# Optimization experiments

Hardware: AMD Instinct MI355X
Metric: run time of the kernel (lower is better)

## Reference

```python
import jax, jax.numpy as jnp
import numpy as np

B, Q, C, N_PER, GS = 8, 2048, 256, 64, 8
H1, H2 = 256, 64
EPS = 1e-5


def make_grid():
    a = jnp.linspace(-0.1, 0.1, GS)
    gx, gy = jnp.meshgrid(a, a, indexing='ij')  # torch.meshgrid default 'ij'
    return jnp.stack([gx.reshape(-1), gy.reshape(-1)], axis=1)  # (n, 2)


def setup_inputs() -> dict:
    key = jax.random.key(0)
    ks = jax.random.split(key, 10)
    s = lambda k, shp, fan: jax.random.normal(k, shp, jnp.float32) / np.sqrt(fan)
    return {
        'tokens': jax.random.normal(ks[0], (B, Q, C), jnp.float32),
        'grid': make_grid(),
        'Wc': s(ks[1], (C, 3), C), 'bc': jnp.zeros((3,), jnp.float32),
        'W1': s(ks[2], (C + 2, H1), C + 2), 'b1': jnp.zeros((H1,), jnp.float32),
        'gamma1': jnp.ones((H1,), jnp.float32), 'beta1': jnp.zeros((H1,), jnp.float32),
        'W2': s(ks[3], (H1, H2), H1), 'b2': jnp.zeros((H2,), jnp.float32),
        'gamma2': jnp.ones((H2,), jnp.float32), 'beta2': jnp.zeros((H2,), jnp.float32),
        'W3': s(ks[4], (H2, 3), H2), 'b3': jnp.zeros((3,), jnp.float32),
    }


def batchnorm(x, gamma, beta):
    # BatchNorm1d in training mode: stats over batch (B*Q) and length (n) dims,
    # per channel (last axis here).
    mean = jnp.mean(x, axis=(0, 1, 2), keepdims=True)
    var = jnp.var(x, axis=(0, 1, 2), keepdims=True)
    return gamma * (x - mean) * jax.lax.rsqrt(var + EPS) + beta


def reference(tokens, grid, Wc, bc, W1, b1, gamma1, beta1, W2, b2, gamma2, beta2, W3, b3):
    coarse = tokens @ Wc + bc  # (B, Q, 3)
    # conv1 (1x1) on concat([tokens_expanded, grid]) == split matmul + broadcast add;
    # avoids materializing the (B,Q,n,C+2) concat explicitly.
    tok_part = tokens @ W1[:C]                 # (B, Q, H1)
    grid_part = grid @ W1[C:]                  # (n, H1)
    h = tok_part[:, :, None, :] + grid_part[None, None, :, :] + b1  # (B, Q, n, H1)
    h = jax.nn.relu(batchnorm(h, gamma1, beta1))
    h = jnp.einsum('bqnc,cd->bqnd', h, W2) + b2  # (B, Q, n, H2)
    h = jax.nn.relu(batchnorm(h, gamma2, beta2))
    disp = jnp.einsum('bqnc,cd->bqnd', h, W3) + b3  # (B, Q, n, 3)
    fine = (coarse[:, :, None, :] + disp).reshape(B, Q * N_PER, 3)
    return coarse, fine
```

## Files before the change

kernel.cpp:

```cpp
#include <hip/hip_runtime.h>
#include <hip/hip_bf16.h>

#define ROWS 16384
#define C_   256
#define H1_  256
#define H2_  64
#define EPSN 1e-5f

typedef __bf16 bf16x8 __attribute__((ext_vector_type(8)));
typedef __bf16 bf16x4 __attribute__((ext_vector_type(4)));
typedef __bf16 bf16x2 __attribute__((ext_vector_type(2)));
typedef float  f32x4  __attribute__((ext_vector_type(4)));
typedef float  f32x2  __attribute__((ext_vector_type(2)));

__device__ __forceinline__ bf16x2 cvt2(float a, float b) {
#if __has_builtin(__builtin_amdgcn_cvt_pk_bf16_f32)
    return __builtin_bit_cast(bf16x2, __builtin_amdgcn_cvt_pk_bf16_f32(a, b));
#else
    bf16x2 r; r[0] = (__bf16)a; r[1] = (__bf16)b; return r;
#endif
}

__device__ __forceinline__ void barrier_lgkm() {
    asm volatile("s_waitcnt lgkmcnt(0)" ::: "memory");
    __builtin_amdgcn_sched_barrier(0);
    __builtin_amdgcn_s_barrier();
    __builtin_amdgcn_sched_barrier(0);
}

__global__ __launch_bounds__(256) void k0_pack(const float* __restrict__ W1,
                                               const float* __restrict__ W2,
                                               const float* __restrict__ W3,
                                               const float* __restrict__ grid,
                                               __bf16* __restrict__ W1p,
                                               __bf16* __restrict__ W2p,
                                               __bf16* __restrict__ W3p,
                                               float* __restrict__ zero_base,
                                               float* __restrict__ gm,
                                               float* __restrict__ gvv) {
    __shared__ float gl[128];
    int idx = blockIdx.x * 256 + threadIdx.x;
    if (idx < 65536) {
        int j = idx & 7, l = (idx >> 3) & 63, rest = idx >> 9;
        int ks = rest & 7, CT = rest >> 3;
        int k = ks * 32 + ((l >> 4) << 3) + j;
        int c = CT * 16 + (l & 15);
        W1p[idx] = (__bf16)W1[k * H1_ + c];
    } else {
        int i2 = idx - 65536;
        int j = i2 & 7, l = (i2 >> 3) & 63, rest = i2 >> 9;
        int ks = rest & 7, CK = rest >> 3;
        int k = ks * 32 + ((l >> 4) << 3) + j;
        int c2 = CK * 16 + (l & 15);
        W2p[i2] = (__bf16)W2[k * H2_ + c2];
    }
    if (idx < 1024) {
        int j = idx & 7, l = (idx >> 3) & 63, ks = idx >> 9;
        int k = ks * 32 + ((l >> 4) << 3) + j;
        int c = l & 15;
        W3p[idx] = (c < 3) ? (__bf16)W3[k * 3 + c] : (__bf16)0.f;
    }
    if (idx < 24576) zero_base[idx] = 0.0f;
    if (blockIdx.x == 0) {
        int t = threadIdx.x;
        if (t < 128) gl[t] = grid[t];
        __syncthreads();
        float wx = W1[C_ * H1_ + t];
        float wy = W1[(C_ + 1) * H1_ + t];
        float mg = 0.f, qg = 0.f;
#pragma unroll
        for (int n = 0; n < 64; ++n) {
            float gv = gl[2 * n] * wx + gl[2 * n + 1] * wy;
            mg += gv; qg = fmaf(gv, gv, qg);
        }
        mg *= (1.f / 64.f);
        gm[t] = mg;
        gvv[t] = qg * (1.f / 64.f) - mg * mg;
    }
}

__device__ __forceinline__ void prep_ctx(const float* __restrict__ grid,
                                         const float* __restrict__ W1,
                                         const float* __restrict__ a1p, int c0,
                                         f32x2* wgx2, f32x2* wgy2, float* A_) {
#pragma unroll
    for (int j = 0; j < 8; ++j) A_[j] = grid[2 * j + 1];
    f32x4 a0 = *(const f32x4*)(a1p + c0), a1h = *(const f32x4*)(a1p + c0 + 4);
    f32x4 x0 = *(const f32x4*)(W1 + C_ * H1_ + c0), x1 = *(const f32x4*)(W1 + C_ * H1_ + c0 + 4);
    f32x4 y0 = *(const f32x4*)(W1 + (C_ + 1) * H1_ + c0), yh = *(const f32x4*)(W1 + (C_ + 1) * H1_ + c0 + 4);
    float av[8] = {a0[0], a0[1], a0[2], a0[3], a1h[0], a1h[1], a1h[2], a1h[3]};
    float wx[8] = {x0[0], x0[1], x0[2], x0[3], x1[0], x1[1], x1[2], x1[3]};
    float wy[8] = {y0[0], y0[1], y0[2], y0[3], yh[0], yh[1], yh[2], yh[3]};
#pragma unroll
    for (int e = 0; e < 4; ++e) {
        wgx2[e][0] = av[2 * e] * wx[2 * e];     wgx2[e][1] = av[2 * e + 1] * wx[2 * e + 1];
        wgy2[e][0] = av[2 * e] * wy[2 * e];     wgy2[e][1] = av[2 * e + 1] * wy[2 * e + 1];
    }
}

__device__ __forceinline__ void stage16(__bf16* __restrict__ y1, int nbase, int c0,
                                        f32x4 a0, f32x4 a1h, f32x4 d0, f32x4 d1h,
                                        const f32x2* wgx2, const f32x2* wgy2,
                                        float ax0, float ax1, f32x4 ay4,
                                        f32x4 t0, f32x4 t1) {
    int chunk = c0 >> 3;
    f32x2 base2[4];
    base2[0][0] = fmaf(a0[0], t0[0], d0[0]);  base2[0][1] = fmaf(a0[1], t0[1], d0[1]);
    base2[1][0] = fmaf(a0[2], t0[2], d0[2]);  base2[1][1] = fmaf(a0[3], t0[3], d0[3]);
    base2[2][0] = fmaf(a1h[0], t1[0], d1h[0]); base2[2][1] = fmaf(a1h[1], t1[1], d1h[1]);
    base2[3][0] = fmaf(a1h[2], t1[2], d1h[2]); base2[3][1] = fmaf(a1h[3], t1[3], d1h[3]);
#pragma unroll
    for (int ih = 0; ih < 2; ++ih) {
        float axs = ih ? ax1 : ax0;
        f32x2 ax2 = {axs, axs};
        f32x2 tc2[4];
#pragma unroll
        for (int e = 0; e < 4; ++e) tc2[e] = __builtin_elementwise_fma(wgx2[e], ax2, base2[e]);
#pragma unroll
        for (int kk = 0; kk < 4; ++kk) {
            float ays = ay4[kk];
            f32x2 ay2 = {ays, ays};
            f32x2 z = {0.f, 0.f};
            int n = nbase + ih * 8 + 2 * kk;
            bf16x8 out;
            bf16x2* o2 = (bf16x2*)&out;
#pragma unroll
            for (int e = 0; e < 4; ++e) {
                f32x2 v = __builtin_elementwise_max(
                    __builtin_elementwise_fma(wgy2[e], ay2, tc2[e]), z);
                o2[e] = cvt2(v[0], v[1]);
            }
            *(bf16x8*)(&y1[n * 256 + ((chunk ^ (n & 7)) << 3)]) = out;
        }
    }
}

__global__ __launch_bounds__(256) void k1a(const float* __restrict__ tokens,
                                           const __bf16* __restrict__ W1p,
                                           const float* __restrict__ Wc,
                                           const float* __restrict__ bc,
                                           float* __restrict__ tokpart,
                                           float* __restrict__ coarse,
                                           float* __restrict__ p1s,
                                           float* __restrict__ p1q) {
    __shared__ __align__(16) __bf16 Al[16 * 264];
    int t = threadIdx.x, w = t >> 6, l = t & 63;
    int quad = l >> 4, col = l & 15;
    int rowbase = (blockIdx.x >> 1) * 16;
    int colhalf = blockIdx.x & 1;
    int slot = blockIdx.x & 31;

    bf16x8 bfr[16];
#pragma unroll
    for (int ctl = 0; ctl < 2; ++ctl)
#pragma unroll
        for (int ks = 0; ks < 8; ++ks) {
            int CT = colhalf * 8 + w * 2 + ctl;
            bfr[ctl * 8 + ks] = *(const bf16x8*)(W1p + (((CT * 8 + ks) * 64 + l) * 8));
        }
    {
        int r = t >> 4, cb = (t & 15) * 16;
        const float* src = tokens + (size_t)(rowbase + r) * C_ + cb;
        f32x4 t0 = *(const f32x4*)(src);
        f32x4 t1 = *(const f32x4*)(src + 4);
        f32x4 t2 = *(const f32x4*)(src + 8);
        f32x4 t3 = *(const f32x4*)(src + 12);
        bf16x8 v0, v1;
        bf16x2* p0 = (bf16x2*)&v0; bf16x2* p1 = (bf16x2*)&v1;
        p0[0] = cvt2(t0[0], t0[1]); p0[1] = cvt2(t0[2], t0[3]);
        p0[2] = cvt2(t1[0], t1[1]); p0[3] = cvt2(t1[2], t1[3]);
        p1[0] = cvt2(t2[0], t2[1]); p1[1] = cvt2(t2[2], t2[3]);
        p1[2] = cvt2(t3[0], t3[1]); p1[3] = cvt2(t3[2], t3[3]);
        *(bf16x8*)(&Al[r * 264 + cb]) = v0;
        *(bf16x8*)(&Al[r * 264 + cb + 8]) = v1;
    }
    barrier_lgkm();

    bf16x8 af[8];
#pragma unroll
    for (int ks = 0; ks < 8; ++ks)
        af[ks] = *(const bf16x8*)(&Al[col * 264 + ks * 32 + quad * 8]);

#pragma unroll
    for (int ctl = 0; ctl < 2; ++ctl) {
        f32x4 acc = {0.f, 0.f, 0.f, 0.f};
#pragma unroll
        for (int ks = 0; ks < 8; ++ks)
            acc = __builtin_amdgcn_mfma_f32_16x16x32_bf16(af[ks], bfr[ctl * 8 + ks], acc, 0, 0, 0);
        int c = colhalf * 128 + w * 32 + ctl * 16 + col;
        float s = 0.f, q = 0.f;
#pragma unroll
        for (int rr = 0; rr < 4; ++rr) {
            float v = acc[rr];
            tokpart[(size_t)(rowbase + quad * 4 + rr) * C_ + c] = v;
            s += v; q += v * v;
        }
        s += __shfl_xor(s, 16, 64); s += __shfl_xor(s, 32, 64);
        q += __shfl_xor(q, 16, 64); q += __shfl_xor(q, 32, 64);
        if (l < 16) {
            int cc = colhalf * 128 + w * 32 + ctl * 16 + l;
            atomicAdd(p1s + slot * C_ + cc, s);
            atomicAdd(p1q + slot * C_ + cc, q);
        }
    }
    if (colhalf == 0) {
        const f32x4* wcp = (const f32x4*)(Wc + l * 12);
        f32x4 wa = wcp[0], wb = wcp[1], wv = wcp[2];
        float wcl[12] = {wa[0], wa[1], wa[2], wa[3], wb[0], wb[1], wb[2], wb[3],
                         wv[0], wv[1], wv[2], wv[3]};
#pragma unroll
        for (int rr = 0; rr < 4; ++rr) {
            int r = w * 4 + rr;
            bf16x4 tv4 = *(const bf16x4*)(&Al[r * 264 + l * 4]);
            float p[3] = {0.f, 0.f, 0.f};
#pragma unroll
            for (int i = 0; i < 4; ++i) {
                float tvf = (float)tv4[i];
#pragma unroll
                for (int j = 0; j < 3; ++j) p[j] = fmaf(tvf, wcl[i * 3 + j], p[j]);
            }
#pragma unroll
            for (int off = 1; off < 64; off <<= 1)
#pragma unroll
                for (int j = 0; j < 3; ++j) p[j] += __shfl_xor(p[j], off, 64);
            if (l == 0) {
#pragma unroll
                for (int j = 0; j < 3; ++j)
                    coarse[(size_t)(rowbase + r) * 3 + j] = p[j] + bc[j];
            }
        }
    }
}

__global__ void k1b(const float* __restrict__ gm, const float* __restrict__ gvv,
                    const float* __restrict__ gamma1, const float* __restrict__ beta1,
                    const float* __restrict__ p1s, const float* __restrict__ p1q,
                    float* __restrict__ a1o, float* __restrict__ d1o) {
    int t = threadIdx.x;
    float S = 0.f, Q = 0.f;
#pragma unroll 8
    for (int s = 0; s < 32; ++s) { S += p1s[s * C_ + t]; Q += p1q[s * C_ + t]; }
    float mean_t = S / (float)ROWS;
    float var_t = Q / (float)ROWS - mean_t * mean_t;
    float a1 = gamma1[t] * rsqrtf(var_t + gvv[t] + EPSN);
    a1o[t] = a1;
    d1o[t] = beta1[t] - a1 * (mean_t + gm[t]);
}

template <bool SPILL>
__global__ __launch_bounds__(256) void k2(const float* __restrict__ tokpart,
                                          const float* __restrict__ grid,
                                          const float* __restrict__ W1,
                                          const __bf16* __restrict__ W2p,
                                          const float* __restrict__ a1,
                                          const float* __restrict__ d1,
                                          float* __restrict__ p2s,
                                          float* __restrict__ p2q,
                                          __bf16* __restrict__ h2s) {
    __shared__ __align__(16) __bf16 y1[2][64 * 256];
    int t = threadIdx.x, w = t >> 6, l = t & 63;
    int quad = l >> 4, col = l & 15;
    int wn = w >> 1, wc = w & 1;
    int c0 = (l & 31) * 8, nh = l >> 5;
    int sw = col & 7;

    bf16x8 bfr[16];
#pragma unroll
    for (int ck = 0; ck < 2; ++ck)
#pragma unroll
        for (int ks = 0; ks < 8; ++ks)
            bfr[ck * 8 + ks] = *(const bf16x8*)(W2p + ((((wc * 2 + ck) * 8 + ks) * 64 + l) * 8));

    f32x2 wgx2[4], wgy2[4]; float A_[8];
    prep_ctx(grid, W1, a1, c0, wgx2, wgy2, A_);

    float ax0 = (w & 2) ? ((w & 1) ? A_[6] : A_[4]) : ((w & 1) ? A_[2] : A_[0]);
    float ax1 = (w & 2) ? ((w & 1) ? A_[7] : A_[5]) : ((w & 1) ? A_[3] : A_[1]);
    f32x4 ay4;
    ay4[0] = nh ? A_[1] : A_[0];
    ay4[1] = nh ? A_[3] : A_[2];
    ay4[2] = nh ? A_[5] : A_[4];
    ay4[3] = nh ? A_[7] : A_[6];
    int nbase = w * 16 + nh;

    f32x4 va0 = *(const f32x4*)(a1 + c0), va1h = *(const f32x4*)(a1 + c0 + 4);
    f32x4 vd0 = *(const f32x4*)(d1 + c0), vd1h = *(const f32x4*)(d1 + c0 + 4);

    float s[2][4] = {}, q[2][4] = {};

    const float* tokbase = tokpart + (size_t)blockIdx.x * 8 * C_;
    {
        f32x4 p0 = *(const f32x4*)(tokbase + c0);
        f32x4 p1 = *(const f32x4*)(tokbase + c0 + 4);
        stage16(&y1[0][0], nbase, c0, va0, va1h, vd0, vd1h, wgx2, wgy2, ax0, ax1, ay4, p0, p1);
    }
    f32x4 t0 = *(const f32x4*)(tokbase + C_ + c0);
    f32x4 t1 = *(const f32x4*)(tokbase + C_ + c0 + 4);
    barrier_lgkm();

#pragma unroll 1
    for (int r8 = 0; r8 < 8; ++r8) {
        int row = blockIdx.x * 8 + r8;
        int cur = r8 & 1;
        int nr = (r8 < 6) ? (r8 + 2) : 7;
        f32x4 n0 = *(const f32x4*)(tokbase + (size_t)nr * C_ + c0);
        f32x4 n1 = *(const f32x4*)(tokbase + (size_t)nr * C_ + c0 + 4);

#pragma unroll
        for (int rt = 0; rt < 2; ++rt) {
            int rowb = (wn * 32 + rt * 16 + col) * 256;
            bf16x8 af[8];
#pragma unroll
            for (int ks = 0; ks < 8; ++ks)
                af[ks] = *(const bf16x8*)(&y1[cur][rowb + (((ks * 4 + quad) ^ sw) << 3)]);
#pragma unroll
            for (int ck = 0; ck < 2; ++ck) {
                f32x4 acc = {0.f, 0.f, 0.f, 0.f};
#pragma unroll
                for (int ks = 0; ks < 8; ++ks)
                    acc = __builtin_amdgcn_mfma_f32_16x16x32_bf16(bfr[ck * 8 + ks], af[ks], acc, 0, 0, 0);
#pragma unroll
                for (int rr = 0; rr < 4; ++rr) {
                    s[ck][rr] += acc[rr];
                    q[ck][rr] += acc[rr] * acc[rr];
                }
                if constexpr (SPILL) {
                    bf16x4 v; bf16x2* v2 = (bf16x2*)&v;
                    v2[0] = cvt2(acc[0], acc[1]);
                    v2[1] = cvt2(acc[2], acc[3]);
                    *(bf16x4*)(h2s + (size_t)row * 4096 +
                               ((wn * 2 + rt) * 4 + wc * 2 + ck) * 256 + l * 4) = v;
                }
            }
        }
        if (r8 < 7)
            stage16(&y1[cur ^ 1][0], nbase, c0, va0, va1h, vd0, vd1h,
                    wgx2, wgy2, ax0, ax1, ay4, t0, t1);
        barrier_lgkm();
        t0 = n0; t1 = n1;
    }
    int slot = ((blockIdx.x << 1) | wn) & 63;
#pragma unroll
    for (int ck = 0; ck < 2; ++ck)
#pragma unroll
        for (int rr = 0; rr < 4; ++rr) {
            float sv = s[ck][rr], qv = q[ck][rr];
            sv += __shfl_xor(sv, 1, 64); sv += __shfl_xor(sv, 2, 64);
            sv += __shfl_xor(sv, 4, 64); sv += __shfl_xor(sv, 8, 64);
            qv += __shfl_xor(qv, 1, 64); qv += __shfl_xor(qv, 2, 64);
            qv += __shfl_xor(qv, 4, 64); qv += __shfl_xor(qv, 8, 64);
            if (col == 0) {
                int c2 = wc * 32 + ck * 16 + quad * 4 + rr;
                atomicAdd(p2s + slot * H2_ + c2, sv);
                atomicAdd(p2q + slot * H2_ + c2, qv);
            }
        }
}

__global__ void k2b(const float* __restrict__ p2s, const float* __restrict__ p2q,
                    const float* __restrict__ gamma2, const float* __restrict__ beta2,
                    float* __restrict__ a2o, float* __restrict__ d2o) {
    int t = threadIdx.x;
    float S = 0.f, Q = 0.f;
#pragma unroll 8
    for (int s = 0; s < 64; ++s) { S += p2s[s * H2_ + t]; Q += p2q[s * H2_ + t]; }
    const float invN = 1.f / ((float)ROWS * 64.f);
    float mean = S * invN;
    float var = Q * invN - mean * mean;
    float a2 = gamma2[t] * rsqrtf(var + EPSN);
    a2o[t] = a2;
    d2o[t] = beta2[t] - a2 * mean;
}

__global__ __launch_bounds__(256) void k3s(const __bf16* __restrict__ h2s,
                                           const float* __restrict__ a2,
                                           const float* __restrict__ d2p,
                                           const __bf16* __restrict__ W3p,
                                           const float* __restrict__ b3,
                                           const float* __restrict__ coarse,
                                           float* __restrict__ fine) {
    __shared__ __align__(16) __bf16 y2l[4][16 * 64];
    __shared__ __align__(16) float finebuf[8 * 192];
    int t = threadIdx.x, w = t >> 6, l = t & 63;
    int quad = l >> 4, col = l & 15;
    int sw = col & 7;

    bf16x8 wfr[2];
#pragma unroll
    for (int ks = 0; ks < 2; ++ks)
        wfr[ks] = *(const bf16x8*)(W3p + ((ks * 64 + l) * 8));

    float a2v[16], d2v[16];
#pragma unroll
    for (int ck = 0; ck < 4; ++ck)
#pragma unroll
        for (int rr = 0; rr < 4; ++rr) {
            int c2 = ck * 16 + quad * 4 + rr;
            a2v[ck * 4 + rr] = a2[c2];
            d2v[ck * 4 + rr] = d2p[c2];
        }
    float b3v = (col < 3) ? b3[col] : 0.f;
    __bf16* yw = &y2l[w][0];

#pragma unroll 1
    for (int r8 = 0; r8 < 8; ++r8) {
        int row = blockIdx.x * 8 + r8;
        const __bf16* src = h2s + (size_t)row * 4096 + l * 4;
        bf16x4 u[4];
#pragma unroll
        for (int ck = 0; ck < 4; ++ck)
            u[ck] = *(const bf16x4*)(src + (w * 4 + ck) * 256);
#pragma unroll
        for (int ck = 0; ck < 4; ++ck) {
            float y0 = fmaxf(fmaf(a2v[ck * 4 + 0], (float)u[ck][0], d2v[ck * 4 + 0]), 0.f);
            float y1v = fmaxf(fmaf(a2v[ck * 4 + 1], (float)u[ck][1], d2v[ck * 4 + 1]), 0.f);
            float y2 = fmaxf(fmaf(a2v[ck * 4 + 2], (float)u[ck][2], d2v[ck * 4 + 2]), 0.f);
            float y3 = fmaxf(fmaf(a2v[ck * 4 + 3], (float)u[ck][3], d2v[ck * 4 + 3]), 0.f);
            bf16x4 v; bf16x2* v2 = (bf16x2*)&v;
            v2[0] = cvt2(y0, y1v); v2[1] = cvt2(y2, y3);
            int chunk = ck * 2 + (quad >> 1);
            *(bf16x4*)(&yw[col * 64 + ((chunk ^ sw) << 3) + (quad & 1) * 4]) = v;
        }
        bf16x8 af2[2];
#pragma unroll
        for (int ks = 0; ks < 2; ++ks)
            af2[ks] = *(const bf16x8*)(&yw[col * 64 + (((ks * 4 + quad) ^ sw) << 3)]);
        f32x4 acc = {0.f, 0.f, 0.f, 0.f};
        acc = __builtin_amdgcn_mfma_f32_16x16x32_bf16(af2[0], wfr[0], acc, 0, 0, 0);
        acc = __builtin_amdgcn_mfma_f32_16x16x32_bf16(af2[1], wfr[1], acc, 0, 0, 0);
        if (col < 3) {
            float cj = coarse[row * 3 + col] + b3v;
#pragma unroll
            for (int rr = 0; rr < 4; ++rr)
                finebuf[r8 * 192 + (w * 16 + quad * 4 + rr) * 3 + col] = acc[rr] + cj;
        }
    }
    __syncthreads();
    {
        float* dst = fine + (size_t)blockIdx.x * 1536;
        const f32x4* fb = (const f32x4*)finebuf;
        *(f32x4*)(dst + 4 * t) = fb[t];
        if (t < 128) *(f32x4*)(dst + 1024 + 4 * t) = fb[256 + t];
    }
}

__global__ __launch_bounds__(256) void k3r(const float* __restrict__ tokpart,
                                           const float* __restrict__ grid,
                                           const float* __restrict__ W1,
                                           const __bf16* __restrict__ W2p,
                                           const float* __restrict__ a1,
                                           const float* __restrict__ d1,
                                           const __bf16* __restrict__ W3p,
                                           const float* __restrict__ a2,
                                           const float* __restrict__ d2p,
                                           const float* __restrict__ b3,
                                           const float* __restrict__ coarse,
                                           float* __restrict__ fine) {
    __shared__ __align__(16) __bf16 y1[64 * 256];
    __shared__ __align__(16) __bf16 y2l[64 * 72];
    __shared__ __align__(16) float finebuf[8 * 192];
    int t = threadIdx.x, w = t >> 6, l = t & 63;
    int quad = l >> 4, col = l & 15;
    int wn = w >> 1, wc = w & 1;
    int c0 = (l & 31) * 8, nh = l >> 5;
    int sw = col & 7;

    bf16x8 bfr[16];
#pragma unroll
    for (int ck = 0; ck < 2; ++ck)
#pragma unroll
        for (int ks = 0; ks < 8; ++ks)
            bfr[ck * 8 + ks] = *(const bf16x8*)(W2p + ((((wc * 2 + ck) * 8 + ks) * 64 + l) * 8));
    bf16x8 wfr[2];
#pragma unroll
    for (int ks = 0; ks < 2; ++ks)
        wfr[ks] = *(const bf16x8*)(W3p + ((ks * 64 + l) * 8));

    f32x2 wgx2[4], wgy2[4]; float A_[8];
    prep_ctx(grid, W1, a1, c0, wgx2, wgy2, A_);

    float ax0 = (w & 2) ? ((w & 1) ? A_[6] : A_[4]) : ((w & 1) ? A_[2] : A_[0]);
    float ax1 = (w & 2) ? ((w & 1) ? A_[7] : A_[5]) : ((w & 1) ? A_[3] : A_[1]);
    f32x4 ay4;
    ay4[0] = nh ? A_[1] : A_[0];
    ay4[1] = nh ? A_[3] : A_[2];
    ay4[2] = nh ? A_[5] : A_[4];
    ay4[3] = nh ? A_[7] : A_[6];
    int nbase = w * 16 + nh;

    f32x4 va0 = *(const f32x4*)(a1 + c0), va1h = *(const f32x4*)(a1 + c0 + 4);
    f32x4 vd0 = *(const f32x4*)(d1 + c0), vd1h = *(const f32x4*)(d1 + c0 + 4);

    float a2v[8], d2v[8];
#pragma unroll
    for (int ck = 0; ck < 2; ++ck)
#pragma unroll
        for (int rr = 0; rr < 4; ++rr) {
            int c2 = wc * 32 + ck * 16 + quad * 4 + rr;
            a2v[ck * 4 + rr] = a2[c2];
            d2v[ck * 4 + rr] = d2p[c2];
        }
    float b3v = (col < 3) ? b3[col] : 0.f;

    const float* tokbase = tokpart + (size_t)blockIdx.x * 8 * C_;
    f32x4 t0 = *(const f32x4*)(tokbase + c0);
    f32x4 t1 = *(const f32x4*)(tokbase + c0 + 4);

#pragma unroll 1
    for (int r8 = 0; r8 < 8; ++r8) {
        int row = blockIdx.x * 8 + r8;
        int nr = (r8 < 7) ? (r8 + 1) : 7;
        f32x4 n0 = *(const f32x4*)(tokbase + (size_t)nr * C_ + c0);
        f32x4 n1 = *(const f32x4*)(tokbase + (size_t)nr * C_ + c0 + 4);

        stage16(y1, nbase, c0, va0, va1h, vd0, vd1h, wgx2, wgy2, ax0, ax1, ay4, t0, t1);
        barrier_lgkm();
#pragma unroll
        for (int rt = 0; rt < 2; ++rt) {
            int rowb = (wn * 32 + rt * 16 + col) * 256;
            bf16x8 af[8];
#pragma unroll
            for (int ks = 0; ks < 8; ++ks)
                af[ks] = *(const bf16x8*)(&y1[rowb + (((ks * 4 + quad) ^ sw) << 3)]);
#pragma unroll
            for (int ck = 0; ck < 2; ++ck) {
                f32x4 acc = {0.f, 0.f, 0.f, 0.f};
#pragma unroll
                for (int ks = 0; ks < 8; ++ks)
                    acc = __builtin_amdgcn_mfma_f32_16x16x32_bf16(bfr[ck * 8 + ks], af[ks], acc, 0, 0, 0);
                bf16x4 v; bf16x2* v2 = (bf16x2*)&v;
                float y0 = fmaxf(fmaf(a2v[ck * 4 + 0], acc[0], d2v[ck * 4 + 0]), 0.f);
                float y1v = fmaxf(fmaf(a2v[ck * 4 + 1], acc[1], d2v[ck * 4 + 1]), 0.f);
                float y2 = fmaxf(fmaf(a2v[ck * 4 + 2], acc[2], d2v[ck * 4 + 2]), 0.f);
                float y3 = fmaxf(fmaf(a2v[ck * 4 + 3], acc[3], d2v[ck * 4 + 3]), 0.f);
                v2[0] = cvt2(y0, y1v); v2[1] = cvt2(y2, y3);
                *(bf16x4*)(&y2l[(wn * 32 + rt * 16 + col) * 72 + wc * 32 + ck * 16 + quad * 4]) = v;
            }
        }
        barrier_lgkm();
        bf16x8 af2[2];
#pragma unroll
        for (int ks = 0; ks < 2; ++ks)
            af2[ks] = *(const bf16x8*)(&y2l[(w * 16 + col) * 72 + ks * 32 + quad * 8]);
        f32x4 d2acc = {0.f, 0.f, 0.f, 0.f};
        d2acc = __builtin_amdgcn_mfma_f32_16x16x32_bf16(af2[0], wfr[0], d2acc, 0, 0, 0);
        d2acc = __builtin_amdgcn_mfma_f32_16x16x32_bf16(af2[1], wfr[1], d2acc, 0, 0, 0);
        if (col < 3) {
            float cj = coarse[row * 3 + col] + b3v;
#pragma unroll
            for (int rr = 0; rr < 4; ++rr)
                finebuf[r8 * 192 + (w * 16 + quad * 4 + rr) * 3 + col] = d2acc[rr] + cj;
        }
        barrier_lgkm();
        t0 = n0; t1 = n1;
    }
    {
        float* dst = fine + (size_t)blockIdx.x * 1536;
        const f32x4* fb = (const f32x4*)finebuf;
        *(f32x4*)(dst + 4 * t) = fb[t];
        if (t < 128) *(f32x4*)(dst + 1024 + 4 * t) = fb[256 + t];
    }
}

extern "C" void kernel_launch(void* const* d_in, const int* in_sizes, int n_in,
                              void* d_out, int out_size, void* d_ws, size_t ws_size,
                              hipStream_t stream) {
    (void)in_sizes; (void)n_in; (void)out_size;
    const float* tokens = (const float*)d_in[0];
    const float* grid   = (const float*)d_in[1];
    const float* Wc     = (const float*)d_in[2];
    const float* bc     = (const float*)d_in[3];
    const float* W1     = (const float*)d_in[4];
    const float* gamma1 = (const float*)d_in[6];
    const float* beta1  = (const float*)d_in[7];
    const float* W2     = (const float*)d_in[8];
    const float* gamma2 = (const float*)d_in[10];
    const float* beta2  = (const float*)d_in[11];
    const float* W3     = (const float*)d_in[12];
    const float* b3     = (const float*)d_in[13];

    char* ws = (char*)d_ws;
    __bf16* W1p     = (__bf16*)(ws);
    __bf16* W2p     = (__bf16*)(ws + 131072);
    float*  p1s     = (float*)(ws + 163840);
    float*  p1q     = (float*)(ws + 196608);
    float*  p2s     = (float*)(ws + 229376);
    float*  p2q     = (float*)(ws + 245760);
    float*  a1      = (float*)(ws + 262144);
    float*  d1      = (float*)(ws + 263168);
    float*  a2      = (float*)(ws + 264192);
    float*  d2p     = (float*)(ws + 264448);
    __bf16* W3p     = (__bf16*)(ws + 264704);
    float*  gm      = (float*)(ws + 266752);
    float*  gvv     = (float*)(ws + 267776);
    float*  tokpart = (float*)(ws + 268800);
    __bf16* h2s     = (__bf16*)(ws + 17046016);

    const size_t SPILL_NEED = 17046016ull + 134217728ull;
    bool spill = ws_size >= SPILL_NEED;

    float* coarse = (float*)d_out;
    float* fine   = (float*)d_out + (size_t)ROWS * 3;

    k0_pack<<<320, 256, 0, stream>>>(W1, W2, W3, grid, W1p, W2p, W3p, p1s, gm, gvv);
    k1a<<<2048, 256, 0, stream>>>(tokens, W1p, Wc, bc, tokpart, coarse, p1s, p1q);
    k1b<<<1, 256, 0, stream>>>(gm, gvv, gamma1, beta1, p1s, p1q, a1, d1);
    if (spill) {
        k2<true><<<ROWS / 8, 256, 0, stream>>>(tokpart, grid, W1, W2p, a1, d1,
                                               p2s, p2q, h2s);
        k2b<<<1, 64, 0, stream>>>(p2s, p2q, gamma2, beta2, a2, d2p);
        k3s<<<ROWS / 8, 256, 0, stream>>>(h2s, a2, d2p, W3p, b3, coarse, fine);
    } else {
        k2<false><<<ROWS / 8, 256, 0, stream>>>(tokpart, grid, W1, W2p, a1, d1,
                                                p2s, p2q, h2s);
        k2b<<<1, 64, 0, stream>>>(p2s, p2q, gamma2, beta2, a2, d2p);
        k3r<<<ROWS / 8, 256, 0, stream>>>(tokpart, grid, W1, W2p, a1, d1,
                                          W3p, a2, d2p, b3, coarse, fine);
    }
}
```

Before: 195.4 us.

## Process 64 rows per k1a block and compute coarse head via MFMA

k1a now handles 64 token rows per block instead of 16, so each block reuses its register-resident W1 fragments across four row groups and the grid shrinks from 2048 to 512 blocks. BN1 partial sums are accumulated in registers across row groups before the atomics, which cuts atomic traffic. The coarse projection (tokens @ Wc) moves from scalar FMAs plus a 64-lane shuffle reduction to an MFMA against a zero-padded bf16 Wc packed in k0_pack. The trade-offs are fewer blocks for latency hiding and larger shared memory per block, and coarse is now computed from bf16-rounded weights.

```diff
diff --git a/kernel.cpp b/kernel.cpp
--- a/kernel.cpp
+++ b/kernel.cpp
@@ -31,10 +31,12 @@
 __global__ __launch_bounds__(256) void k0_pack(const float* __restrict__ W1,
                                                const float* __restrict__ W2,
                                                const float* __restrict__ W3,
+                                               const float* __restrict__ Wc,
                                                const float* __restrict__ grid,
                                                __bf16* __restrict__ W1p,
                                                __bf16* __restrict__ W2p,
                                                __bf16* __restrict__ W3p,
+                                               __bf16* __restrict__ Wcp,
                                                float* __restrict__ zero_base,
                                                float* __restrict__ gm,
                                                float* __restrict__ gvv) {
@@ -60,6 +62,12 @@
         int c = l & 15;
         W3p[idx] = (c < 3) ? (__bf16)W3[k * 3 + c] : (__bf16)0.f;
     }
+    if (idx < 4096) {
+        int j = idx & 7, l = (idx >> 3) & 63, ks = idx >> 9;
+        int k = ks * 32 + ((l >> 4) << 3) + j;
+        int c = l & 15;
+        Wcp[idx] = (c < 3) ? (__bf16)Wc[k * 3 + c] : (__bf16)0.f;
+    }
     if (idx < 24576) zero_base[idx] = 0.0f;
     if (blockIdx.x == 0) {
         int t = threadIdx.x;
@@ -137,17 +145,18 @@
 
 __global__ __launch_bounds__(256) void k1a(const float* __restrict__ tokens,
                                            const __bf16* __restrict__ W1p,
-                                           const float* __restrict__ Wc,
+                                           const __bf16* __restrict__ Wcp,
                                            const float* __restrict__ bc,
                                            float* __restrict__ tokpart,
                                            float* __restrict__ coarse,
                                            float* __restrict__ p1s,
                                            float* __restrict__ p1q) {
-    __shared__ __align__(16) __bf16 Al[16 * 264];
+    __shared__ __align__(16) __bf16 Al[64 * 264];
     int t = threadIdx.x, w = t >> 6, l = t & 63;
     int quad = l >> 4, col = l & 15;
-    int rowbase = (blockIdx.x >> 1) * 16;
+    int group = blockIdx.x >> 1;
     int colhalf = blockIdx.x & 1;
+    int rowbase = group * 64;
     int slot = blockIdx.x & 31;
 
     bf16x8 bfr[16];
@@ -158,8 +167,17 @@
             int CT = colhalf * 8 + w * 2 + ctl;
             bfr[ctl * 8 + ks] = *(const bf16x8*)(W1p + (((CT * 8 + ks) * 64 + l) * 8));
         }
-    {
-        int r = t >> 4, cb = (t & 15) * 16;
+    bf16x8 cfr[8];
+    if (colhalf == 0) {
+#pragma unroll
+        for (int ks = 0; ks < 8; ++ks)
+            cfr[ks] = *(const bf16x8*)(Wcp + ((ks * 64 + l) * 8));
+    }
+    float bcv = (col < 3) ? bc[col] : 0.f;
+
+#pragma unroll
+    for (int rg = 0; rg < 4; ++rg) {
+        int r = rg * 16 + (t >> 4), cb = (t & 15) * 16;
         const float* src = tokens + (size_t)(rowbase + r) * C_ + cb;
         f32x4 t0 = *(const f32x4*)(src);
         f32x4 t1 = *(const f32x4*)(src + 4);
@@ -176,58 +194,52 @@
     }
     barrier_lgkm();
 
-    bf16x8 af[8];
-#pragma unroll
-    for (int ks = 0; ks < 8; ++ks)
-        af[ks] = *(const bf16x8*)(&Al[col * 264 + ks * 32 + quad * 8]);
+    float s[2] = {0.f, 0.f}, q[2] = {0.f, 0.f};
+
+#pragma unroll
+    for (int rg = 0; rg < 4; ++rg) {
+        int rb16 = rg * 16;
+        bf16x8 af[8];
+#pragma unroll
+        for (int ks = 0; ks < 8; ++ks)
+            af[ks] = *(const bf16x8*)(&Al[(rb16 + col) * 264 + ks * 32 + quad * 8]);
+
+#pragma unroll
+        for (int ctl = 0; ctl < 2; ++ctl) {
+            f32x4 acc = {0.f, 0.f, 0.f, 0.f};
+#pragma unroll
+            for (int ks = 0; ks < 8; ++ks)
+                acc = __builtin_amdgcn_mfma_f32_16x16x32_bf16(af[ks], bfr[ctl * 8 + ks], acc, 0, 0, 0);
+            int c = colhalf * 128 + w * 32 + ctl * 16 + col;
+#pragma unroll
+            for (int rr = 0; rr < 4; ++rr) {
+                float v = acc[rr];
+                tokpart[(size_t)(rowbase + rb16 + quad * 4 + rr) * C_ + c] = v;
+                s[ctl] += v; q[ctl] += v * v;
+            }
+        }
+        if (colhalf == 0) {
+            f32x4 cacc = {0.f, 0.f, 0.f, 0.f};
+#pragma unroll
+            for (int ks = 0; ks < 8; ++ks)
+                cacc = __builtin_amdgcn_mfma_f32_16x16x32_bf16(af[ks], cfr[ks], cacc, 0, 0, 0);
+            if (col < 3) {
+#pragma unroll
+                for (int rr = 0; rr < 4; ++rr)
+                    coarse[(size_t)(rowbase + rb16 + quad * 4 + rr) * 3 + col] = cacc[rr] + bcv;
+            }
+        }
+    }
 
 #pragma unroll
     for (int ctl = 0; ctl < 2; ++ctl) {
-        f32x4 acc = {0.f, 0.f, 0.f, 0.f};
-#pragma unroll
-        for (int ks = 0; ks < 8; ++ks)
-            acc = __builtin_amdgcn_mfma_f32_16x16x32_bf16(af[ks], bfr[ctl * 8 + ks], acc, 0, 0, 0);
-        int c = colhalf * 128 + w * 32 + ctl * 16 + col;
-        float s = 0.f, q = 0.f;
-#pragma unroll
-        for (int rr = 0; rr < 4; ++rr) {
-            float v = acc[rr];
-            tokpart[(size_t)(rowbase + quad * 4 + rr) * C_ + c] = v;
-            s += v; q += v * v;
-        }
-        s += __shfl_xor(s, 16, 64); s += __shfl_xor(s, 32, 64);
-        q += __shfl_xor(q, 16, 64); q += __shfl_xor(q, 32, 64);
+        float sv = s[ctl], qv = q[ctl];
+        sv += __shfl_xor(sv, 16, 64); sv += __shfl_xor(sv, 32, 64);
+        qv += __shfl_xor(qv, 16, 64); qv += __shfl_xor(qv, 32, 64);
         if (l < 16) {
             int cc = colhalf * 128 + w * 32 + ctl * 16 + l;
-            atomicAdd(p1s + slot * C_ + cc, s);
-            atomicAdd(p1q + slot * C_ + cc, q);
-        }
-    }
-    if (colhalf == 0) {
-        const f32x4* wcp = (const f32x4*)(Wc + l * 12);
-        f32x4 wa = wcp[0], wb = wcp[1], wv = wcp[2];
-        float wcl[12] = {wa[0], wa[1], wa[2], wa[3], wb[0], wb[1], wb[2], wb[3],
-                         wv[0], wv[1], wv[2], wv[3]};
-#pragma unroll
-        for (int rr = 0; rr < 4; ++rr) {
-            int r = w * 4 + rr;
-            bf16x4 tv4 = *(const bf16x4*)(&Al[r * 264 + l * 4]);
-            float p[3] = {0.f, 0.f, 0.f};
-#pragma unroll
-            for (int i = 0; i < 4; ++i) {
-                float tvf = (float)tv4[i];
-#pragma unroll
-                for (int j = 0; j < 3; ++j) p[j] = fmaf(tvf, wcl[i * 3 + j], p[j]);
-            }
-#pragma unroll
-            for (int off = 1; off < 64; off <<= 1)
-#pragma unroll
-                for (int j = 0; j < 3; ++j) p[j] += __shfl_xor(p[j], off, 64);
-            if (l == 0) {
-#pragma unroll
-                for (int j = 0; j < 3; ++j)
-                    coarse[(size_t)(rowbase + r) * 3 + j] = p[j] + bc[j];
-            }
+            atomicAdd(p1s + slot * C_ + cc, sv);
+            atomicAdd(p1q + slot * C_ + cc, qv);
         }
     }
 }
@@ -591,19 +603,21 @@
     float*  a2      = (float*)(ws + 264192);
     float*  d2p     = (float*)(ws + 264448);
     __bf16* W3p     = (__bf16*)(ws + 264704);
-    float*  gm      = (float*)(ws + 266752);
-    float*  gvv     = (float*)(ws + 267776);
-    float*  tokpart = (float*)(ws + 268800);
-    __bf16* h2s     = (__bf16*)(ws + 17046016);
-
-    const size_t SPILL_NEED = 17046016ull + 134217728ull;
+    __bf16* Wcp     = (__bf16*)(ws + 266752);
+    float*  gm      = (float*)(ws + 274944);
+    float*  gvv     = (float*)(ws + 275968);
+    float*  tokpart = (float*)(ws + 276992);
+    __bf16* h2s     = (__bf16*)(ws + 17054208);
+
+    const size_t SPILL_NEED = 17054208ull + 134217728ull;
     bool spill = ws_size >= SPILL_NEED;
 
     float* coarse = (float*)d_out;
     float* fine   = (float*)d_out + (size_t)ROWS * 3;
 
-    k0_pack<<<320, 256, 0, stream>>>(W1, W2, W3, grid, W1p, W2p, W3p, p1s, gm, gvv);
-    k1a<<<2048, 256, 0, stream>>>(tokens, W1p, Wc, bc, tokpart, coarse, p1s, p1q);
+    k0_pack<<<320, 256, 0, stream>>>(W1, W2, W3, Wc, grid, W1p, W2p, W3p, Wcp,
+                                     p1s, gm, gvv);
+    k1a<<<512, 256, 0, stream>>>(tokens, W1p, Wcp, bc, tokpart, coarse, p1s, p1q);
     k1b<<<1, 256, 0, stream>>>(gm, gvv, gamma1, beta1, p1s, p1q, a1, d1);
     if (spill) {
         k2<true><<<ROWS / 8, 256, 0, stream>>>(tokpart, grid, W1, W2p, a1, d1,
```

New measurement: 191.1 us. 1.02x faster.
